# Kernel tuning notes

Measured on AMD Instinct MI355X. Metric: run time of the kernel, lower is better.

## Reference

```python
import jax, jax.numpy as jnp
import numpy as np

DIM = 2048
DIM_HEAD = 128
HEADS = 16
FF_MULT = 4
ATTN_INNER = DIM_HEAD * HEADS          # 2048
FF_INNER = DIM * FF_MULT               # 8192
FUSED = ATTN_INNER + DIM_HEAD + DIM_HEAD + 2 * FF_INNER  # 18688


def setup_inputs() -> dict:
    key = jax.random.key(0)
    k1, k2, k3, k4 = jax.random.split(key, 4)
    B, N = 2, 2048
    x = jax.random.normal(k1, (B, N, DIM), dtype=jnp.float32)
    gamma = jnp.ones((DIM,), dtype=jnp.float32)
    w_fused = jax.random.normal(k2, (DIM, FUSED), dtype=jnp.float32) * 0.02
    w_attn_out = jax.random.normal(k3, (ATTN_INNER, DIM), dtype=jnp.float32) * 0.02
    w_ff_out = jax.random.normal(k4, (FF_INNER, DIM), dtype=jnp.float32) * 0.02
    return {"x": x, "gamma": gamma, "w_fused": w_fused,
            "w_attn_out": w_attn_out, "w_ff_out": w_ff_out}


def _rotate_half(t):
    d = t.shape[-1] // 2
    x1, x2 = t[..., :d], t[..., d:]
    return jnp.concatenate((-x2, x1), axis=-1)


def _apply_rope(pos, t):
    return t * jnp.cos(pos) + _rotate_half(t) * jnp.sin(pos)


def reference(x, gamma, w_fused, w_attn_out, w_ff_out):
    B, N, _ = x.shape
    # LayerNorm (beta fixed at zero)
    mu = jnp.mean(x, axis=-1, keepdims=True)
    var = jnp.var(x, axis=-1, keepdims=True)
    xn = (x - mu) / jnp.sqrt(var + 1e-5) * gamma

    proj = xn @ w_fused  # [B, N, FUSED]
    q = proj[..., :ATTN_INNER]
    k = proj[..., ATTN_INNER:ATTN_INNER + DIM_HEAD]
    v = proj[..., ATTN_INNER + DIM_HEAD:ATTN_INNER + 2 * DIM_HEAD]
    ff = proj[..., ATTN_INNER + 2 * DIM_HEAD:]

    q = q.reshape(B, N, HEADS, DIM_HEAD).transpose(0, 2, 1, 3)  # b h n d

    # rotary positions: [N, DIM_HEAD]
    inv_freq = 1.0 / (10000.0 ** (jnp.arange(0, DIM_HEAD, 2, dtype=jnp.float32) / DIM_HEAD))
    freqs = jnp.arange(N, dtype=jnp.float32)[:, None] * inv_freq[None, :]
    pos = jnp.concatenate((freqs, freqs), axis=-1)

    q = _apply_rope(pos, q)
    k = _apply_rope(pos, k)
    q = q * (DIM_HEAD ** -0.5)

    sim = jnp.einsum('bhid,bjd->bhij', q, k)  # multi-query: shared k head
    neg = -jnp.finfo(sim.dtype).max
    causal = jnp.triu(jnp.ones((N, N), dtype=bool), 1)
    sim = jnp.where(causal, neg, sim)
    sim = sim - jax.lax.stop_gradient(jnp.max(sim, axis=-1, keepdims=True))
    attn = jax.nn.softmax(sim, axis=-1)
    out = jnp.einsum('bhij,bjd->bhid', attn, v)
    out = out.transpose(0, 2, 1, 3).reshape(B, N, ATTN_INNER)

    # SwiGLU feedforward
    ff_x, gate = ff[..., :FF_INNER], ff[..., FF_INNER:]
    ff_out = (jax.nn.silu(gate) * ff_x) @ w_ff_out

    return out @ w_attn_out + ff_out
```

## Files before the change

### kernel.cpp

```cpp
#include <hip/hip_runtime.h>
#include <hip/hip_bf16.h>

typedef __attribute__((ext_vector_type(4))) float f32x4;
typedef __attribute__((ext_vector_type(8))) __bf16 bf16x8;

#define DIMC 2048
#define NSEQ 2048
#define BATCH 2
#define HEADSC 16
#define DHEAD 128
#define ATTN_IN 2048
#define FF_IN 8192
#define FUSED_COLS 18688
#define ROWS 4096
#define KCAT 10240

constexpr size_t OFF_XN   = 0;
constexpr size_t OFF_Q    = 16777216;
constexpr size_t OFF_K    = 33554432;
constexpr size_t OFF_VT   = 34603008;
constexpr size_t OFF_ACAT = 35651584;
constexpr size_t OFF_GATE = 119537664;
constexpr size_t OFF_WFT  = 186646528;
constexpr size_t OFF_WCT  = 263192576;

__global__ __launch_bounds__(256) void ln_kernel(const float* __restrict__ x,
                                                 const float* __restrict__ gamma,
                                                 __hip_bfloat16* __restrict__ xn) {
  int row = blockIdx.x;
  int tid = threadIdx.x;
  int lane = tid & 63, wave = tid >> 6;
  const float4* xr = (const float4*)(x + (size_t)row * DIMC);
  float4 a = xr[tid], b = xr[tid + 256];
  float s  = a.x + a.y + a.z + a.w + b.x + b.y + b.z + b.w;
  float ss = a.x*a.x + a.y*a.y + a.z*a.z + a.w*a.w + b.x*b.x + b.y*b.y + b.z*b.z + b.w*b.w;
  #pragma unroll
  for (int o = 32; o; o >>= 1) { s += __shfl_down(s, o); ss += __shfl_down(ss, o); }
  __shared__ float red[8];
  if (lane == 0) { red[wave] = s; red[4 + wave] = ss; }
  __syncthreads();
  s  = red[0] + red[1] + red[2] + red[3];
  ss = red[4] + red[5] + red[6] + red[7];
  float mean = s * (1.f / DIMC);
  float var  = ss * (1.f / DIMC) - mean * mean;
  float rstd = rsqrtf(var + 1e-5f);
  const float4* gp = (const float4*)gamma;
  float4 g1 = gp[tid], g2 = gp[tid + 256];
  __hip_bfloat16* o = xn + (size_t)row * DIMC;
  o[tid*4+0]      = __float2bfloat16((a.x - mean) * rstd * g1.x);
  o[tid*4+1]      = __float2bfloat16((a.y - mean) * rstd * g1.y);
  o[tid*4+2]      = __float2bfloat16((a.z - mean) * rstd * g1.z);
  o[tid*4+3]      = __float2bfloat16((a.w - mean) * rstd * g1.w);
  o[1024+tid*4+0] = __float2bfloat16((b.x - mean) * rstd * g2.x);
  o[1024+tid*4+1] = __float2bfloat16((b.y - mean) * rstd * g2.y);
  o[1024+tid*4+2] = __float2bfloat16((b.z - mean) * rstd * g2.z);
  o[1024+tid*4+3] = __float2bfloat16((b.w - mean) * rstd * g2.w);
}

__global__ __launch_bounds__(256) void transpose_bf16(const float* __restrict__ src,
                                                      __hip_bfloat16* __restrict__ dst,
                                                      int R, int C, int dstStride, int dstOff) {
  __shared__ __align__(16) __hip_bfloat16 tile[64][72];
  int c0 = blockIdx.x * 64, r0 = blockIdx.y * 64;
  int tx = threadIdx.x & 15;
  int ty = threadIdx.x >> 4;
  #pragma unroll
  for (int i = 0; i < 64; i += 16) {
    float4 v = *(const float4*)(src + (size_t)(r0 + ty + i) * C + c0 + tx * 4);
    tile[tx*4+0][ty+i] = __float2bfloat16(v.x);
    tile[tx*4+1][ty+i] = __float2bfloat16(v.y);
    tile[tx*4+2][ty+i] = __float2bfloat16(v.z);
    tile[tx*4+3][ty+i] = __float2bfloat16(v.w);
  }
  __syncthreads();
  int rx = (threadIdx.x & 7) * 8;
  #pragma unroll
  for (int i = 0; i < 64; i += 32) {
    int cc = (threadIdx.x >> 3) + i;
    *(bf16x8*)(dst + (size_t)(c0 + cc) * dstStride + dstOff + r0 + rx) = *(const bf16x8*)&tile[cc][rx];
  }
}

struct GemmP {
  const __hip_bfloat16* A;
  const __hip_bfloat16* B;
  int K;
  int kTilesPer;
  int nbx;
  int nmn;
  int cpx;
  __hip_bfloat16* outF0;
  __hip_bfloat16* outF1;
  int Nout;
  __hip_bfloat16 *q, *kk, *vT, *acat, *gate;
};

#define LDA_Q(BUFIDX, QM) { \
    const char* slot_ = lds + ((BUFIDX) << 16) + ((QM) << 14); \
    _Pragma("unroll") for (int mi = 0; mi < 4; ++mi) \
    _Pragma("unroll") for (int ks = 0; ks < 2; ++ks) { \
      int row_ = (mi << 5) + (wr << 4) + (lane & 15); \
      int ch_  = (ks << 2) + (lane >> 4); \
      af[mi][ks] = *(const bf16x8*)(slot_ + (row_ << 7) + ((ch_ ^ (row_ & 7)) << 4)); } }

#define LDB_Q(DST, BUFIDX, QN) { \
    const char* slot_ = lds + ((BUFIDX) << 16) + 32768 + ((QN) << 14); \
    _Pragma("unroll") for (int ni = 0; ni < 2; ++ni) \
    _Pragma("unroll") for (int ks = 0; ks < 2; ++ks) { \
      int row_ = (ni << 6) + (wn << 4) + (lane & 15); \
      int ch_  = (ks << 2) + (lane >> 4); \
      DST[ni][ks] = *(const bf16x8*)(slot_ + (row_ << 7) + ((ch_ ^ (row_ & 7)) << 4)); } }

#define DO_MFMA_Q(QM, BSET, QN) \
    __builtin_amdgcn_s_setprio(1); \
    _Pragma("unroll") for (int mi = 0; mi < 4; ++mi) \
    _Pragma("unroll") for (int ni = 0; ni < 2; ++ni) \
    _Pragma("unroll") for (int ks = 0; ks < 2; ++ks) \
      acc[(QM)*4+mi][(QN)*2+ni] = __builtin_amdgcn_mfma_f32_16x16x32_bf16( \
          af[mi][ks], BSET[ni][ks], acc[(QM)*4+mi][(QN)*2+ni], 0, 0, 0); \
    __builtin_amdgcn_s_setprio(0);

#define KTILE_BODY(KT, BUFC) \
    LDB_Q(b0r, BUFC, 0); \
    LDA_Q(BUFC, 0); \
    stage(Bb, (KT) + 1, 1, 0); \
    asm volatile("s_waitcnt lgkmcnt(8)"); \
    __builtin_amdgcn_s_barrier(); \
    asm volatile("s_waitcnt lgkmcnt(0)"); \
    __builtin_amdgcn_sched_barrier(0); \
    DO_MFMA_Q(0, b0r, 0); \
    __builtin_amdgcn_s_barrier(); \
    LDB_Q(b1r, BUFC, 1); \
    stage(Bb, (KT) + 1, 1, 1); \
    __builtin_amdgcn_s_barrier(); \
    asm volatile("s_waitcnt lgkmcnt(0)"); \
    __builtin_amdgcn_sched_barrier(0); \
    DO_MFMA_Q(0, b1r, 1); \
    __builtin_amdgcn_s_barrier(); \
    LDA_Q(BUFC, 1); \
    stage(Ab, (KT) + 2, 0, 0); \
    __builtin_amdgcn_s_barrier(); \
    asm volatile("s_waitcnt lgkmcnt(0)"); \
    __builtin_amdgcn_sched_barrier(0); \
    DO_MFMA_Q(1, b0r, 0); \
    __builtin_amdgcn_s_barrier(); \
    stage(Ab, (KT) + 2, 0, 1); \
    asm volatile("s_waitcnt vmcnt(4)" ::: "memory"); \
    __builtin_amdgcn_sched_barrier(0); \
    __builtin_amdgcn_s_barrier(); \
    DO_MFMA_Q(1, b1r, 1);

template<int EPI>
__global__ __launch_bounds__(512, 2) void gemm256(GemmP p) {
  __shared__ __align__(16) char lds[131072];
  const int tid = threadIdx.x;
  const int lane = tid & 63, wave = tid >> 6;
  const int wr = wave >> 2, wn = wave & 3;

  int l = ((int)blockIdx.x & 7) * p.cpx + ((int)blockIdx.x >> 3);
  int kp = l / p.nmn;
  int r = l - kp * p.nmn;
  int per = 8 * p.nbx;
  int g = r / per;
  int rg = r - g * per;
  int by = (g << 3) + (rg & 7);
  int bx = rg >> 3;
  int m0 = by << 8, n0 = bx << 8;

  const int NT = p.kTilesPer;
  const size_t Kb = (size_t)p.K * 2;
  const size_t koff = (size_t)kp * NT * 128;
  const char* Ab = (const char*)p.A + (size_t)m0 * Kb + koff;
  const char* Bb = (const char*)p.B + (size_t)n0 * Kb + koff;

  auto stage = [&](const char* mbase, int ktTgt, int isB, int h) {
    int ks = ktTgt < NT ? ktTgt : NT - 1;
    char* dst = lds + ((ktTgt & 1) << 16) + (isB << 15) + (h << 14);
    #pragma unroll
    for (int j = 0; j < 2; ++j) {
      int c = (j << 9) + tid;
      int row = c >> 3;
      int gl = ((c & 7) ^ (row & 7)) << 4;
      __builtin_amdgcn_global_load_lds(
        (const __attribute__((address_space(1))) void*)(mbase + (size_t)((h << 7) + row) * Kb + (size_t)ks * 128 + gl),
        (__attribute__((address_space(3))) void*)(dst + (c << 4)), 16, 0, 0);
    }
  };

  bf16x8 af[4][2], b0r[2][2], b1r[2][2];
  f32x4 acc[8][4] = {};

  stage(Ab, 0, 0, 0); stage(Ab, 0, 0, 1);
  stage(Bb, 0, 1, 0); stage(Bb, 0, 1, 1);
  stage(Ab, 1, 0, 0); stage(Ab, 1, 0, 1);
  asm volatile("s_waitcnt vmcnt(4)" ::: "memory");
  __builtin_amdgcn_sched_barrier(0);
  __builtin_amdgcn_s_barrier();

  for (int kt = 0; kt < NT; kt += 2) {
    KTILE_BODY(kt, 0);
    KTILE_BODY(kt + 1, 1);
  }

  asm volatile("s_waitcnt vmcnt(0) lgkmcnt(0)" ::: "memory");

  if constexpr (EPI == 1) {
    #pragma unroll
    for (int mig = 0; mig < 8; ++mig) {
      int rr0 = m0 + (mig << 5) + (wr << 4) + ((lane >> 4) << 2);
      #pragma unroll
      for (int nig = 0; nig < 4; ++nig) {
        int cc = n0 + (nig << 6) + (wn << 4) + (lane & 15);
        #pragma unroll
        for (int rr_ = 0; rr_ < 4; ++rr_) {
          int rr = rr0 + rr_;
          int b = rr >> 11, n = rr & 2047;
          __hip_bfloat16 hv = __float2bfloat16(acc[mig][nig][rr_]);
          if (cc < 2048) {
            int h = cc >> 7, d = cc & 127;
            p.q[((((size_t)b << 4) + h) * NSEQ + n) * DHEAD + d] = hv;
          } else if (cc < 2176) {
            p.kk[(size_t)rr * DHEAD + (cc - 2048)] = hv;
          } else if (cc < 2304) {
            p.vT[(((size_t)b << 7) + (cc - 2176)) * NSEQ + n] = hv;
          } else if (cc < 10496) {
            p.acat[(size_t)rr * KCAT + (cc - 256)] = hv;
          } else {
            p.gate[(size_t)rr * FF_IN + (cc - 10496)] = hv;
          }
        }
      }
    }
  } else {
    __hip_bfloat16* dst = kp ? p.outF1 : p.outF0;
    #pragma unroll
    for (int mig = 0; mig < 8; ++mig) {
      int rr0 = m0 + (mig << 5) + (wr << 4) + ((lane >> 4) << 2);
      #pragma unroll
      for (int nig = 0; nig < 4; ++nig) {
        int cc = n0 + (nig << 6) + (wn << 4) + (lane & 15);
        #pragma unroll
        for (int rr_ = 0; rr_ < 4; ++rr_)
          dst[(size_t)(rr0 + rr_) * p.Nout + cc] = __float2bfloat16(acc[mig][nig][rr_]);
      }
    }
  }
}

__global__ __launch_bounds__(256) void addout_kernel(const __hip_bfloat16* __restrict__ a,
                                                     const __hip_bfloat16* __restrict__ b,
                                                     float* __restrict__ o, int n8) {
  int i = blockIdx.x * 256 + threadIdx.x;
  if (i < n8) {
    bf16x8 x = ((const bf16x8*)a)[i], y = ((const bf16x8*)b)[i];
    float4 o1, o2;
    o1.x = (float)x[0] + (float)y[0]; o1.y = (float)x[1] + (float)y[1];
    o1.z = (float)x[2] + (float)y[2]; o1.w = (float)x[3] + (float)y[3];
    o2.x = (float)x[4] + (float)y[4]; o2.y = (float)x[5] + (float)y[5];
    o2.z = (float)x[6] + (float)y[6]; o2.w = (float)x[7] + (float)y[7];
    ((float4*)o)[i * 2]     = o1;
    ((float4*)o)[i * 2 + 1] = o2;
  }
}

__global__ __launch_bounds__(256) void rope_kernel(__hip_bfloat16* __restrict__ t,
                                                   int totalRows, float scale) {
  int idx = blockIdx.x * 256 + threadIdx.x;
  if (idx >= totalRows * 64) return;
  int i = idx & 63;
  int row = idx >> 6;
  int n = row & (NSEQ - 1);
  float f = __expf(-(float)i * 0.14391157f);
  float ang = (float)n * f;
  float sv, cv;
  sincosf(ang, &sv, &cv);
  __hip_bfloat16* pp = t + (size_t)row * DHEAD;
  float x1 = __bfloat162float(pp[i]);
  float x2 = __bfloat162float(pp[i + 64]);
  pp[i]      = __float2bfloat16((x1 * cv - x2 * sv) * scale);
  pp[i + 64] = __float2bfloat16((x2 * cv + x1 * sv) * scale);
}

__global__ __launch_bounds__(256, 2) void attn_part_kernel(const __hip_bfloat16* __restrict__ q,
                                                           const __hip_bfloat16* __restrict__ k,
                                                           const __hip_bfloat16* __restrict__ vT,
                                                           __hip_bfloat16* __restrict__ opart,
                                                           float* __restrict__ mpart,
                                                           float* __restrict__ lpart) {
  __shared__ __align__(16) char alds[81920];
  char* Ktile = alds;
  char* Vtile = alds + 32768;
  char* Pb    = alds + 65536;
  const int tid = threadIdx.x;
  int c = 79 - (int)blockIdx.x;
  int bh = blockIdx.y;
  int qt, ch;
  if (c < 8)       { qt = c;                 ch = 0; }
  else if (c < 24) { qt = 8  + ((c - 8) >> 1);  ch = (c - 8) & 1; }
  else if (c < 48) { qt = 16 + (c - 24) / 3;    ch = (c - 24) % 3; }
  else             { qt = 24 + ((c - 48) >> 2); ch = (c - 48) & 3; }
  int slot = bh * 80 + c;
  int b = bh >> 4;
  int lane = tid & 63, wave = tid >> 6;
  int q0 = qt << 6;
  int qrow0 = q0 + (wave << 4);
  const __hip_bfloat16* qbase = q + (size_t)bh * NSEQ * DHEAD;
  const char* kbase = (const char*)(k + (size_t)b * NSEQ * DHEAD);
  const char* vbase = (const char*)(vT + (size_t)b * DHEAD * NSEQ);
  char* Pw = Pb + (wave << 12);

  auto stageK = [&](int j0) {
    const char* kb = kbase + (size_t)j0 * 256;
    #pragma unroll
    for (int it = 0; it < 8; ++it) {
      int s = (it << 8) + tid;
      int row = s >> 4, cch = s & 15;
      int sch = (cch & 8) | ((cch & 7) ^ (row & 7));
      __builtin_amdgcn_global_load_lds(
        (const __attribute__((address_space(1))) void*)(kb + (size_t)row * 256 + (sch << 4)),
        (__attribute__((address_space(3))) void*)(Ktile + (s << 4)), 16, 0, 0);
    }
  };
  auto stageV = [&](int j0) {
    const char* vb = vbase + (size_t)j0 * 2;
    #pragma unroll
    for (int it = 0; it < 8; ++it) {
      int s = (it << 8) + tid;
      int row = s >> 4, cch = s & 15;
      int sch = (cch & 8) | ((cch & 7) ^ (row & 7));
      __builtin_amdgcn_global_load_lds(
        (const __attribute__((address_space(1))) void*)(vb + (size_t)row * (NSEQ * 2) + (sch << 4)),
        (__attribute__((address_space(3))) void*)(Vtile + (s << 4)), 16, 0, 0);
    }
  };

  bf16x8 qf[4];
  #pragma unroll
  for (int ks = 0; ks < 4; ++ks)
    qf[ks] = *(const bf16x8*)(qbase + (size_t)(qrow0 + (lane & 15)) * DHEAD + (ks << 5) + ((lane >> 4) << 3));
  {
    const float SCALE = 0.08838834764831845f;
    float nrow = (float)(qrow0 + (lane & 15));
    #pragma unroll
    for (int ks = 0; ks < 2; ++ks) {
      #pragma unroll
      for (int j = 0; j < 8; ++j) {
        int d = (ks << 5) + ((lane >> 4) << 3) + j;
        float f = __expf(-(float)d * 0.14391157f);
        float sv, cv;
        sincosf(nrow * f, &sv, &cv);
        float x1 = (float)qf[ks][j];
        float x2 = (float)qf[ks + 2][j];
        qf[ks][j]     = (__bf16)((x1 * cv - x2 * sv) * SCALE);
        qf[ks + 2][j] = (__bf16)((x2 * cv + x1 * sv) * SCALE);
      }
    }
  }
  f32x4 o[8] = {};
  float mrow[4] = {-1e30f, -1e30f, -1e30f, -1e30f};
  float lrow[4] = {0.f, 0.f, 0.f, 0.f};
  int nTiles = (q0 + 64 + 127) >> 7;
  int jBeg = ch << 2;
  int jEnd = jBeg + 4 < nTiles ? jBeg + 4 : nTiles;

  stageK(jBeg << 7);
  stageV(jBeg << 7);
  asm volatile("s_waitcnt vmcnt(0)" ::: "memory");
  __builtin_amdgcn_s_barrier();

  for (int j2 = jBeg; j2 < jEnd; ++j2) {
    int j0 = j2 << 7;
    bool more = (j2 + 1 < jEnd);
    f32x4 s[8] = {};
    #pragma unroll
    for (int ks = 0; ks < 4; ++ks) {
      bf16x8 kf2[8];
      #pragma unroll
      for (int nf = 0; nf < 8; ++nf) {
        int row_ = (nf << 4) + (lane & 15);
        int ch_  = (ks << 2) + (lane >> 4);
        int sch  = (ch_ & 8) | ((ch_ & 7) ^ (row_ & 7));
        kf2[nf] = *(const bf16x8*)(Ktile + (row_ << 8) + (sch << 4));
      }
      __builtin_amdgcn_s_setprio(1);
      #pragma unroll
      for (int nf = 0; nf < 8; ++nf)
        s[nf] = __builtin_amdgcn_mfma_f32_16x16x32_bf16(qf[ks], kf2[nf], s[nf], 0, 0, 0);
      __builtin_amdgcn_s_setprio(0);
    }
    __builtin_amdgcn_s_barrier();
    if (more) stageK((j0 + 128));
    if (j0 + 127 > q0) {
      #pragma unroll
      for (int nf = 0; nf < 8; ++nf) {
        int cg = j0 + (nf << 4) + (lane & 15);
        #pragma unroll
        for (int r = 0; r < 4; ++r) {
          int rg = qrow0 + ((lane >> 4) << 2) + r;
          if (cg > rg) s[nf][r] = -1e30f;
        }
      }
    }
    float tm[4] = {-1e30f, -1e30f, -1e30f, -1e30f};
    #pragma unroll
    for (int nf = 0; nf < 8; ++nf)
      #pragma unroll
      for (int r = 0; r < 4; ++r) tm[r] = fmaxf(tm[r], s[nf][r]);
    #pragma unroll
    for (int r = 0; r < 4; ++r) {
      #pragma unroll
      for (int msk = 1; msk < 16; msk <<= 1)
        tm[r] = fmaxf(tm[r], __shfl_xor(tm[r], msk));
    }
    float scl[4], ps[4] = {0.f, 0.f, 0.f, 0.f};
    #pragma unroll
    for (int r = 0; r < 4; ++r) {
      float mn = fmaxf(mrow[r], tm[r]);
      scl[r] = __expf(mrow[r] - mn);
      mrow[r] = mn;
    }
    #pragma unroll
    for (int nf = 0; nf < 8; ++nf) {
      #pragma unroll
      for (int r = 0; r < 4; ++r) {
        float pv = __expf(s[nf][r] - mrow[r]);
        ps[r] += pv;
        int prow = ((lane >> 4) << 2) + r;
        int pcol = (nf << 4) + (lane & 15);
        int pch  = pcol >> 3;
        int psch = (pch & 8) | ((pch & 7) ^ (prow & 7));
        *(__hip_bfloat16*)(Pw + (prow << 8) + (psch << 4) + ((pcol & 7) << 1)) = __float2bfloat16(pv);
      }
    }
    #pragma unroll
    for (int r = 0; r < 4; ++r) {
      #pragma unroll
      for (int msk = 1; msk < 16; msk <<= 1) ps[r] += __shfl_xor(ps[r], msk);
      lrow[r] = lrow[r] * scl[r] + ps[r];
    }
    #pragma unroll
    for (int df = 0; df < 8; ++df)
      #pragma unroll
      for (int r = 0; r < 4; ++r) o[df][r] *= scl[r];
    #pragma unroll
    for (int ks2 = 0; ks2 < 4; ++ks2) {
      int prow = lane & 15;
      int pch  = (ks2 << 2) + (lane >> 4);
      int psch = (pch & 8) | ((pch & 7) ^ (prow & 7));
      bf16x8 pf = *(const bf16x8*)(Pw + (prow << 8) + (psch << 4));
      bf16x8 vf2[8];
      #pragma unroll
      for (int df = 0; df < 8; ++df) {
        int row_ = (df << 4) + (lane & 15);
        int ch_  = (ks2 << 2) + (lane >> 4);
        int sch  = (ch_ & 8) | ((ch_ & 7) ^ (row_ & 7));
        vf2[df] = *(const bf16x8*)(Vtile + (row_ << 8) + (sch << 4));
      }
      __builtin_amdgcn_s_setprio(1);
      #pragma unroll
      for (int df = 0; df < 8; ++df)
        o[df] = __builtin_amdgcn_mfma_f32_16x16x32_bf16(pf, vf2[df], o[df], 0, 0, 0);
      __builtin_amdgcn_s_setprio(0);
    }
    if (more) {
      __builtin_amdgcn_s_barrier();
      stageV(j0 + 128);
      asm volatile("s_waitcnt vmcnt(0)" ::: "memory");
      __builtin_amdgcn_s_barrier();
    }
  }
  size_t rbase = ((size_t)slot << 6) + (wave << 4) + ((lane >> 4) << 2);
  #pragma unroll
  for (int df = 0; df < 8; ++df)
    #pragma unroll
    for (int r = 0; r < 4; ++r)
      opart[(rbase + r) * 128 + (df << 4) + (lane & 15)] = __float2bfloat16(o[df][r]);
  if ((lane & 15) == 0) {
    #pragma unroll
    for (int r = 0; r < 4; ++r) { mpart[rbase + r] = mrow[r]; lpart[rbase + r] = lrow[r]; }
  }
}

__global__ __launch_bounds__(256) void attn_comb_kernel(const __hip_bfloat16* __restrict__ opart,
                                                        const float* __restrict__ mpart,
                                                        const float* __restrict__ lpart,
                                                        __hip_bfloat16* __restrict__ acat) {
  int t = blockIdx.x * 256 + threadIdx.x;
  int dg = t & 15;
  int rg = (t >> 4) & 2047;
  int bh = t >> 15;
  int qt = rg >> 6;
  int nc = (qt + 8) >> 3;
  int S = qt;
  if (qt >= 8)  S += qt - 8;
  if (qt >= 16) S += qt - 16;
  if (qt >= 24) S += qt - 24;
  size_t base = (((size_t)bh * 80 + S) << 6) + (rg & 63);
  float M = -1e30f;
  for (int cc = 0; cc < nc; ++cc) M = fmaxf(M, mpart[base + ((size_t)cc << 6)]);
  float O[8] = {};
  float L = 0.f;
  for (int cc = 0; cc < nc; ++cc) {
    size_t rb = base + ((size_t)cc << 6);
    float w = __expf(mpart[rb] - M);
    L += w * lpart[rb];
    bf16x8 ov = *(const bf16x8*)(opart + rb * 128 + (dg << 3));
    #pragma unroll
    for (int j = 0; j < 8; ++j) O[j] += w * (float)ov[j];
  }
  float invL = 1.f / L;
  int b = bh >> 4, h = bh & 15;
  bf16x8 res;
  #pragma unroll
  for (int j = 0; j < 8; ++j) res[j] = (__bf16)(O[j] * invL);
  *(bf16x8*)(acat + ((size_t)(b * 2048 + rg)) * KCAT + (h << 7) + (dg << 3)) = res;
}

__global__ __launch_bounds__(256) void silu_kernel(__hip_bfloat16* __restrict__ acat,
                                                   const __hip_bfloat16* __restrict__ gate) {
  size_t idx = ((size_t)blockIdx.x * 256 + threadIdx.x) << 3;
  int r = (int)(idx >> 13);
  int j = (int)(idx & 8191);
  bf16x8 g = *(const bf16x8*)(gate + idx);
  size_t ai = (size_t)r * KCAT + 2048 + j;
  bf16x8 fx = *(const bf16x8*)(acat + ai);
  bf16x8 res;
  #pragma unroll
  for (int t = 0; t < 8; ++t) {
    float gf = (float)g[t];
    res[t] = (__bf16)((float)fx[t] * gf / (1.f + __expf(-gf)));
  }
  *(bf16x8*)(acat + ai) = res;
}

extern "C" void kernel_launch(void* const* d_in, const int* in_sizes, int n_in,
                              void* d_out, int out_size, void* d_ws, size_t ws_size,
                              hipStream_t stream) {
  (void)in_sizes; (void)n_in; (void)out_size; (void)ws_size;
  const float* x          = (const float*)d_in[0];
  const float* gamma      = (const float*)d_in[1];
  const float* w_fused    = (const float*)d_in[2];
  const float* w_attn_out = (const float*)d_in[3];
  const float* w_ff_out   = (const float*)d_in[4];
  char* ws = (char*)d_ws;
  __hip_bfloat16* xn    = (__hip_bfloat16*)(ws + OFF_XN);
  __hip_bfloat16* qbuf  = (__hip_bfloat16*)(ws + OFF_Q);
  __hip_bfloat16* kbuf  = (__hip_bfloat16*)(ws + OFF_K);
  __hip_bfloat16* vTbuf = (__hip_bfloat16*)(ws + OFF_VT);
  __hip_bfloat16* acat  = (__hip_bfloat16*)(ws + OFF_ACAT);
  __hip_bfloat16* gateb = (__hip_bfloat16*)(ws + OFF_GATE);
  __hip_bfloat16* wfT   = (__hip_bfloat16*)(ws + OFF_WFT);
  __hip_bfloat16* wcT   = (__hip_bfloat16*)(ws + OFF_WCT);
  __hip_bfloat16* P0 = (__hip_bfloat16*)(ws + OFF_XN);
  __hip_bfloat16* P1 = (__hip_bfloat16*)(ws + OFF_GATE);
  __hip_bfloat16* oPart = (__hip_bfloat16*)(ws + OFF_WFT);
  float* mPart = (float*)(ws + OFF_XN);
  float* lPart = (float*)(ws + OFF_XN + 1048576);

  transpose_bf16<<<dim3(FUSED_COLS / 64, DIMC / 64), 256, 0, stream>>>(w_fused, wfT, DIMC, FUSED_COLS, DIMC, 0);
  transpose_bf16<<<dim3(DIMC / 64, DIMC / 64), 256, 0, stream>>>(w_attn_out, wcT, ATTN_IN, DIMC, KCAT, 0);
  transpose_bf16<<<dim3(DIMC / 64, FF_IN / 64), 256, 0, stream>>>(w_ff_out, wcT, FF_IN, DIMC, KCAT, ATTN_IN);

  ln_kernel<<<ROWS, 256, 0, stream>>>(x, gamma, xn);

  GemmP g1;
  g1.A = xn; g1.B = wfT; g1.K = DIMC; g1.kTilesPer = DIMC / 64;
  g1.nbx = FUSED_COLS / 256; g1.nmn = (FUSED_COLS / 256) * (ROWS / 256);
  g1.cpx = g1.nmn / 8;
  g1.outF0 = nullptr; g1.outF1 = nullptr; g1.Nout = 0;
  g1.q = qbuf; g1.kk = kbuf; g1.vT = vTbuf; g1.acat = acat; g1.gate = gateb;
  gemm256<1><<<g1.nmn, 512, 0, stream>>>(g1);

  rope_kernel<<<(BATCH * NSEQ * 64) / 256, 256, 0, stream>>>(kbuf, BATCH * NSEQ, 1.0f);

  attn_part_kernel<<<dim3(80, BATCH * HEADSC), 256, 0, stream>>>(qbuf, kbuf, vTbuf, oPart, mPart, lPart);
  attn_comb_kernel<<<(BATCH * HEADSC * NSEQ * DHEAD / 8) / 256, 256, 0, stream>>>(oPart, mPart, lPart, acat);

  silu_kernel<<<(int)(((size_t)ROWS * FF_IN / 8) / 256), 256, 0, stream>>>(acat, gateb);

  GemmP g2;
  g2.A = acat; g2.B = wcT; g2.K = KCAT; g2.kTilesPer = (KCAT / 64) / 2;
  g2.nbx = DIMC / 256; g2.nmn = (DIMC / 256) * (ROWS / 256);
  g2.cpx = (g2.nmn * 2) / 8;
  g2.outF0 = P0; g2.outF1 = P1; g2.Nout = DIMC;
  g2.q = nullptr; g2.kk = nullptr; g2.vT = nullptr; g2.acat = nullptr; g2.gate = nullptr;
  gemm256<3><<<g2.nmn * 2, 512, 0, stream>>>(g2);

  addout_kernel<<<(ROWS * DIMC / 8 + 255) / 256, 256, 0, stream>>>(P0, P1, (float*)d_out, ROWS * DIMC / 8);
}
```

Measured before the change: 695.8 us.

## Double query rows per attention block and pipeline K/V staging

Each wave now handles 32 query rows in two 16-row fragments, so a block covers 128 queries and each K/V tile loaded into LDS feeds twice the MFMA work. The grid shrinks from 80 to 40 chunks per head, and the combine kernel's chunk indexing is updated to match. K/V prefetch now waits with a partial vmcnt and always issues a clamped next-tile load, so loads overlap compute instead of draining fully. P is written and consumed in two halves to fit the LDS buffer. This raises register pressure and halves the number of blocks, which may reduce occupancy or load balance.

Result: slower. 763.4 us (+9.7%).

```diff
diff --git a/kernel.cpp b/kernel.cpp
--- a/kernel.cpp
+++ b/kernel.cpp
@@ -292,25 +292,30 @@
   char* Vtile = alds + 32768;
   char* Pb    = alds + 65536;
   const int tid = threadIdx.x;
-  int c = 79 - (int)blockIdx.x;
+  int c = 39 - (int)blockIdx.x;
   int bh = blockIdx.y;
   int qt, ch;
-  if (c < 8)       { qt = c;                 ch = 0; }
-  else if (c < 24) { qt = 8  + ((c - 8) >> 1);  ch = (c - 8) & 1; }
-  else if (c < 48) { qt = 16 + (c - 24) / 3;    ch = (c - 24) % 3; }
-  else             { qt = 24 + ((c - 48) >> 2); ch = (c - 48) & 3; }
-  int slot = bh * 80 + c;
+  if (c < 4)       { qt = c;                  ch = 0; }
+  else if (c < 12) { qt = 4  + ((c - 4) >> 1);  ch = (c - 4) & 1; }
+  else if (c < 24) { qt = 8  + (c - 12) / 3;    ch = (c - 12) % 3; }
+  else             { qt = 12 + ((c - 24) >> 2); ch = (c - 24) & 3; }
+  int slot = bh * 40 + c;
   int b = bh >> 4;
   int lane = tid & 63, wave = tid >> 6;
-  int q0 = qt << 6;
-  int qrow0 = q0 + (wave << 4);
+  int q0 = qt << 7;
+  int qrow0 = q0 + (wave << 5);
   const __hip_bfloat16* qbase = q + (size_t)bh * NSEQ * DHEAD;
   const char* kbase = (const char*)(k + (size_t)b * NSEQ * DHEAD);
   const char* vbase = (const char*)(vT + (size_t)b * DHEAD * NSEQ);
   char* Pw = Pb + (wave << 12);
 
-  auto stageK = [&](int j0) {
-    const char* kb = kbase + (size_t)j0 * 256;
+  int nT = qt + 1;
+  int jBeg = ch << 2;
+  int jEnd = jBeg + 4 < nT ? jBeg + 4 : nT;
+
+  auto stageK = [&](int j2) {
+    int jc = j2 < jEnd ? j2 : jEnd - 1;
+    const char* kb = kbase + (size_t)(jc << 7) * 256;
     #pragma unroll
     for (int it = 0; it < 8; ++it) {
       int s = (it << 8) + tid;
@@ -321,8 +326,9 @@
         (__attribute__((address_space(3))) void*)(Ktile + (s << 4)), 16, 0, 0);
     }
   };
-  auto stageV = [&](int j0) {
-    const char* vb = vbase + (size_t)j0 * 2;
+  auto stageV = [&](int j2) {
+    int jc = j2 < jEnd ? j2 : jEnd - 1;
+    const char* vb = vbase + (size_t)(jc << 7) * 2;
     #pragma unroll
     for (int it = 0; it < 8; ++it) {
       int s = (it << 8) + tid;
@@ -334,13 +340,16 @@
     }
   };
 
-  bf16x8 qf[4];
+  bf16x8 qf0[4], qf1[4];
   #pragma unroll
-  for (int ks = 0; ks < 4; ++ks)
-    qf[ks] = *(const bf16x8*)(qbase + (size_t)(qrow0 + (lane & 15)) * DHEAD + (ks << 5) + ((lane >> 4) << 3));
+  for (int ks = 0; ks < 4; ++ks) {
+    qf0[ks] = *(const bf16x8*)(qbase + (size_t)(qrow0 + (lane & 15)) * DHEAD + (ks << 5) + ((lane >> 4) << 3));
+    qf1[ks] = *(const bf16x8*)(qbase + (size_t)(qrow0 + 16 + (lane & 15)) * DHEAD + (ks << 5) + ((lane >> 4) << 3));
+  }
   {
     const float SCALE = 0.08838834764831845f;
-    float nrow = (float)(qrow0 + (lane & 15));
+    float n0f = (float)(qrow0 + (lane & 15));
+    float n1f = n0f + 16.f;
     #pragma unroll
     for (int ks = 0; ks < 2; ++ks) {
       #pragma unroll
@@ -348,30 +357,30 @@
         int d = (ks << 5) + ((lane >> 4) << 3) + j;
         float f = __expf(-(float)d * 0.14391157f);
         float sv, cv;
-        sincosf(nrow * f, &sv, &cv);
-        float x1 = (float)qf[ks][j];
-        float x2 = (float)qf[ks + 2][j];
-        qf[ks][j]     = (__bf16)((x1 * cv - x2 * sv) * SCALE);
-        qf[ks + 2][j] = (__bf16)((x2 * cv + x1 * sv) * SCALE);
-      }
-    }
-  }
-  f32x4 o[8] = {};
-  float mrow[4] = {-1e30f, -1e30f, -1e30f, -1e30f};
-  float lrow[4] = {0.f, 0.f, 0.f, 0.f};
-  int nTiles = (q0 + 64 + 127) >> 7;
-  int jBeg = ch << 2;
-  int jEnd = jBeg + 4 < nTiles ? jBeg + 4 : nTiles;
-
-  stageK(jBeg << 7);
-  stageV(jBeg << 7);
-  asm volatile("s_waitcnt vmcnt(0)" ::: "memory");
+        sincosf(n0f * f, &sv, &cv);
+        float x1 = (float)qf0[ks][j], x2 = (float)qf0[ks + 2][j];
+        qf0[ks][j]     = (__bf16)((x1 * cv - x2 * sv) * SCALE);
+        qf0[ks + 2][j] = (__bf16)((x2 * cv + x1 * sv) * SCALE);
+        sincosf(n1f * f, &sv, &cv);
+        float y1 = (float)qf1[ks][j], y2 = (float)qf1[ks + 2][j];
+        qf1[ks][j]     = (__bf16)((y1 * cv - y2 * sv) * SCALE);
+        qf1[ks + 2][j] = (__bf16)((y2 * cv + y1 * sv) * SCALE);
+      }
+    }
+  }
+
+  f32x4 o0[8] = {}, o1[8] = {};
+  float m0r[4] = {-1e30f, -1e30f, -1e30f, -1e30f}, m1r[4] = {-1e30f, -1e30f, -1e30f, -1e30f};
+  float l0r[4] = {0.f, 0.f, 0.f, 0.f}, l1r[4] = {0.f, 0.f, 0.f, 0.f};
+
+  stageK(jBeg);
+  stageV(jBeg);
+  asm volatile("s_waitcnt vmcnt(8)" ::: "memory");
   __builtin_amdgcn_s_barrier();
 
   for (int j2 = jBeg; j2 < jEnd; ++j2) {
     int j0 = j2 << 7;
-    bool more = (j2 + 1 < jEnd);
-    f32x4 s[8] = {};
+    f32x4 s0[8] = {}, s1[8] = {};
     #pragma unroll
     for (int ks = 0; ks < 4; ++ks) {
       bf16x8 kf2[8];
@@ -385,99 +394,130 @@
       __builtin_amdgcn_s_setprio(1);
       #pragma unroll
       for (int nf = 0; nf < 8; ++nf)
-        s[nf] = __builtin_amdgcn_mfma_f32_16x16x32_bf16(qf[ks], kf2[nf], s[nf], 0, 0, 0);
+        s0[nf] = __builtin_amdgcn_mfma_f32_16x16x32_bf16(qf0[ks], kf2[nf], s0[nf], 0, 0, 0);
+      #pragma unroll
+      for (int nf = 0; nf < 8; ++nf)
+        s1[nf] = __builtin_amdgcn_mfma_f32_16x16x32_bf16(qf1[ks], kf2[nf], s1[nf], 0, 0, 0);
       __builtin_amdgcn_s_setprio(0);
     }
     __builtin_amdgcn_s_barrier();
-    if (more) stageK((j0 + 128));
+    stageK(j2 + 1);
+    asm volatile("s_waitcnt vmcnt(8)" ::: "memory");
+    __builtin_amdgcn_s_barrier();
     if (j0 + 127 > q0) {
       #pragma unroll
       for (int nf = 0; nf < 8; ++nf) {
         int cg = j0 + (nf << 4) + (lane & 15);
         #pragma unroll
         for (int r = 0; r < 4; ++r) {
-          int rg = qrow0 + ((lane >> 4) << 2) + r;
-          if (cg > rg) s[nf][r] = -1e30f;
+          int rg0 = qrow0 + ((lane >> 4) << 2) + r;
+          if (cg > rg0) s0[nf][r] = -1e30f;
+          if (cg > rg0 + 16) s1[nf][r] = -1e30f;
         }
       }
     }
-    float tm[4] = {-1e30f, -1e30f, -1e30f, -1e30f};
+    float tm0[4] = {-1e30f, -1e30f, -1e30f, -1e30f}, tm1[4] = {-1e30f, -1e30f, -1e30f, -1e30f};
     #pragma unroll
     for (int nf = 0; nf < 8; ++nf)
       #pragma unroll
-      for (int r = 0; r < 4; ++r) tm[r] = fmaxf(tm[r], s[nf][r]);
+      for (int r = 0; r < 4; ++r) { tm0[r] = fmaxf(tm0[r], s0[nf][r]); tm1[r] = fmaxf(tm1[r], s1[nf][r]); }
     #pragma unroll
     for (int r = 0; r < 4; ++r) {
       #pragma unroll
-      for (int msk = 1; msk < 16; msk <<= 1)
-        tm[r] = fmaxf(tm[r], __shfl_xor(tm[r], msk));
-    }
-    float scl[4], ps[4] = {0.f, 0.f, 0.f, 0.f};
+      for (int msk = 1; msk < 16; msk <<= 1) {
+        tm0[r] = fmaxf(tm0[r], __shfl_xor(tm0[r], msk));
+        tm1[r] = fmaxf(tm1[r], __shfl_xor(tm1[r], msk));
+      }
+    }
+    float sc0[4], sc1[4], ps0[4] = {}, ps1[4] = {};
     #pragma unroll
     for (int r = 0; r < 4; ++r) {
-      float mn = fmaxf(mrow[r], tm[r]);
-      scl[r] = __expf(mrow[r] - mn);
-      mrow[r] = mn;
+      float mn0 = fmaxf(m0r[r], tm0[r]);
+      sc0[r] = __expf(m0r[r] - mn0); m0r[r] = mn0;
+      float mn1 = fmaxf(m1r[r], tm1[r]);
+      sc1[r] = __expf(m1r[r] - mn1); m1r[r] = mn1;
     }
     #pragma unroll
     for (int nf = 0; nf < 8; ++nf) {
       #pragma unroll
       for (int r = 0; r < 4; ++r) {
-        float pv = __expf(s[nf][r] - mrow[r]);
-        ps[r] += pv;
-        int prow = ((lane >> 4) << 2) + r;
-        int pcol = (nf << 4) + (lane & 15);
-        int pch  = pcol >> 3;
-        int psch = (pch & 8) | ((pch & 7) ^ (prow & 7));
-        *(__hip_bfloat16*)(Pw + (prow << 8) + (psch << 4) + ((pcol & 7) << 1)) = __float2bfloat16(pv);
+        float p0 = __expf(s0[nf][r] - m0r[r]); ps0[r] += p0; s0[nf][r] = p0;
+        float p1 = __expf(s1[nf][r] - m1r[r]); ps1[r] += p1; s1[nf][r] = p1;
       }
     }
     #pragma unroll
     for (int r = 0; r < 4; ++r) {
       #pragma unroll
-      for (int msk = 1; msk < 16; msk <<= 1) ps[r] += __shfl_xor(ps[r], msk);
-      lrow[r] = lrow[r] * scl[r] + ps[r];
+      for (int msk = 1; msk < 16; msk <<= 1) { ps0[r] += __shfl_xor(ps0[r], msk); ps1[r] += __shfl_xor(ps1[r], msk); }
+      l0r[r] = l0r[r] * sc0[r] + ps0[r];
+      l1r[r] = l1r[r] * sc1[r] + ps1[r];
     }
     #pragma unroll
     for (int df = 0; df < 8; ++df)
       #pragma unroll
-      for (int r = 0; r < 4; ++r) o[df][r] *= scl[r];
-    #pragma unroll
-    for (int ks2 = 0; ks2 < 4; ++ks2) {
-      int prow = lane & 15;
-      int pch  = (ks2 << 2) + (lane >> 4);
-      int psch = (pch & 8) | ((pch & 7) ^ (prow & 7));
-      bf16x8 pf = *(const bf16x8*)(Pw + (prow << 8) + (psch << 4));
-      bf16x8 vf2[8];
-      #pragma unroll
-      for (int df = 0; df < 8; ++df) {
-        int row_ = (df << 4) + (lane & 15);
-        int ch_  = (ks2 << 2) + (lane >> 4);
-        int sch  = (ch_ & 8) | ((ch_ & 7) ^ (row_ & 7));
-        vf2[df] = *(const bf16x8*)(Vtile + (row_ << 8) + (sch << 4));
-      }
-      __builtin_amdgcn_s_setprio(1);
-      #pragma unroll
-      for (int df = 0; df < 8; ++df)
-        o[df] = __builtin_amdgcn_mfma_f32_16x16x32_bf16(pf, vf2[df], o[df], 0, 0, 0);
-      __builtin_amdgcn_s_setprio(0);
-    }
-    if (more) {
-      __builtin_amdgcn_s_barrier();
-      stageV(j0 + 128);
-      asm volatile("s_waitcnt vmcnt(0)" ::: "memory");
-      __builtin_amdgcn_s_barrier();
-    }
-  }
-  size_t rbase = ((size_t)slot << 6) + (wave << 4) + ((lane >> 4) << 2);
+      for (int r = 0; r < 4; ++r) { o0[df][r] *= sc0[r]; o1[df][r] *= sc1[r]; }
+    #pragma unroll
+    for (int half = 0; half < 2; ++half) {
+      #pragma unroll
+      for (int nf4 = 0; nf4 < 4; ++nf4) {
+        int nf = (half << 2) + nf4;
+        int col = (nf4 << 4) + (lane & 15);
+        int pch = col >> 3, inb = (col & 7) << 1;
+        #pragma unroll
+        for (int r = 0; r < 4; ++r) {
+          int prow = ((lane >> 4) << 2) + r;
+          int psch = pch ^ (prow & 7);
+          *(__hip_bfloat16*)(Pw + (prow << 7) + (psch << 4) + inb) = __float2bfloat16(s0[nf][r]);
+          *(__hip_bfloat16*)(Pw + 2048 + (prow << 7) + (psch << 4) + inb) = __float2bfloat16(s1[nf][r]);
+        }
+      }
+      #pragma unroll
+      for (int k2 = 0; k2 < 2; ++k2) {
+        int ks2 = (half << 1) + k2;
+        int prow = lane & 15;
+        int pch = (k2 << 2) + (lane >> 4);
+        int psch = pch ^ (prow & 7);
+        bf16x8 pf0 = *(const bf16x8*)(Pw + (prow << 7) + (psch << 4));
+        bf16x8 pf1 = *(const bf16x8*)(Pw + 2048 + (prow << 7) + (psch << 4));
+        bf16x8 vf2[8];
+        #pragma unroll
+        for (int df = 0; df < 8; ++df) {
+          int row_ = (df << 4) + (lane & 15);
+          int ch_  = (ks2 << 2) + (lane >> 4);
+          int sch  = (ch_ & 8) | ((ch_ & 7) ^ (row_ & 7));
+          vf2[df] = *(const bf16x8*)(Vtile + (row_ << 8) + (sch << 4));
+        }
+        __builtin_amdgcn_s_setprio(1);
+        #pragma unroll
+        for (int df = 0; df < 8; ++df)
+          o0[df] = __builtin_amdgcn_mfma_f32_16x16x32_bf16(pf0, vf2[df], o0[df], 0, 0, 0);
+        #pragma unroll
+        for (int df = 0; df < 8; ++df)
+          o1[df] = __builtin_amdgcn_mfma_f32_16x16x32_bf16(pf1, vf2[df], o1[df], 0, 0, 0);
+        __builtin_amdgcn_s_setprio(0);
+      }
+    }
+    __builtin_amdgcn_s_barrier();
+    stageV(j2 + 1);
+    asm volatile("s_waitcnt vmcnt(8)" ::: "memory");
+    __builtin_amdgcn_s_barrier();
+  }
+  asm volatile("s_waitcnt vmcnt(0)" ::: "memory");
+
+  size_t rb0 = ((size_t)slot << 7) + (wave << 5) + ((lane >> 4) << 2);
   #pragma unroll
   for (int df = 0; df < 8; ++df)
     #pragma unroll
-    for (int r = 0; r < 4; ++r)
-      opart[(rbase + r) * 128 + (df << 4) + (lane & 15)] = __float2bfloat16(o[df][r]);
+    for (int r = 0; r < 4; ++r) {
+      opart[(rb0 + r) * 128 + (df << 4) + (lane & 15)] = __float2bfloat16(o0[df][r]);
+      opart[(rb0 + 16 + r) * 128 + (df << 4) + (lane & 15)] = __float2bfloat16(o1[df][r]);
+    }
   if ((lane & 15) == 0) {
     #pragma unroll
-    for (int r = 0; r < 4; ++r) { mpart[rbase + r] = mrow[r]; lpart[rbase + r] = lrow[r]; }
+    for (int r = 0; r < 4; ++r) {
+      mpart[rb0 + r] = m0r[r];      lpart[rb0 + r] = l0r[r];
+      mpart[rb0 + 16 + r] = m1r[r]; lpart[rb0 + 16 + r] = l1r[r];
+    }
   }
 }
 
@@ -489,19 +529,20 @@
   int dg = t & 15;
   int rg = (t >> 4) & 2047;
   int bh = t >> 15;
-  int qt = rg >> 6;
-  int nc = (qt + 8) >> 3;
-  int S = qt;
-  if (qt >= 8)  S += qt - 8;
-  if (qt >= 16) S += qt - 16;
-  if (qt >= 24) S += qt - 24;
-  size_t base = (((size_t)bh * 80 + S) << 6) + (rg & 63);
+  int qt = rg >> 7;
+  int nc = (qt >> 2) + 1;
+  int S;
+  if (qt < 4)       S = qt;
+  else if (qt < 8)  S = 4 + 2 * (qt - 4);
+  else if (qt < 12) S = 12 + 3 * (qt - 8);
+  else              S = 24 + 4 * (qt - 12);
+  size_t base = (((size_t)bh * 40 + S) << 7) + (rg & 127);
   float M = -1e30f;
-  for (int cc = 0; cc < nc; ++cc) M = fmaxf(M, mpart[base + ((size_t)cc << 6)]);
+  for (int cc = 0; cc < nc; ++cc) M = fmaxf(M, mpart[base + ((size_t)cc << 7)]);
   float O[8] = {};
   float L = 0.f;
   for (int cc = 0; cc < nc; ++cc) {
-    size_t rb = base + ((size_t)cc << 6);
+    size_t rb = base + ((size_t)cc << 7);
     float w = __expf(mpart[rb] - M);
     L += w * lpart[rb];
     bf16x8 ov = *(const bf16x8*)(opart + rb * 128 + (dg << 3));
@@ -573,7 +614,7 @@
 
   rope_kernel<<<(BATCH * NSEQ * 64) / 256, 256, 0, stream>>>(kbuf, BATCH * NSEQ, 1.0f);
 
-  attn_part_kernel<<<dim3(80, BATCH * HEADSC), 256, 0, stream>>>(qbuf, kbuf, vTbuf, oPart, mPart, lPart);
+  attn_part_kernel<<<dim3(40, BATCH * HEADSC), 256, 0, stream>>>(qbuf, kbuf, vTbuf, oPart, mPart, lPart);
   attn_comb_kernel<<<(BATCH * HEADSC * NSEQ * DHEAD / 8) / 256, 256, 0, stream>>>(oPart, mPart, lPart, acat);
 
   silu_kernel<<<(int)(((size_t)ROWS * FF_IN / 8) / 256), 256, 0, stream>>>(acat, gateb);
```
